# Kernel tuning notes

Hardware: AMD Instinct MI355X
Metric: run time of the kernel (lower is better)

The kernel has to match this reference:

```python
import jax, jax.numpy as jnp
import numpy as np

DELTA = 10.0
EPS = 1e-08
THRESHOLD = 0.9
STEEPNESS = 10.0


def setup_inputs() -> dict:
    key = jax.random.key(0)
    k1, k2 = jax.random.split(key)
    B, T2, T1, F = 16, 2048, 512, 128
    mels = jax.random.normal(k1, (B, T2, F), dtype=jnp.float32)
    alpha = jax.random.uniform(k2, (B, T2, T1), dtype=jnp.float32)
    mel_mask = jnp.ones((B, T2), dtype=jnp.int32)
    text_mask = jnp.ones((B, T1), dtype=jnp.int32)
    return {"mels": mels, "alpha": alpha, "mel_mask": mel_mask, "text_mask": text_mask}


def reference(mels, alpha, mel_mask, text_mask):
    B, T2, F = mels.shape
    T1 = text_mask.shape[-1]
    audio_mask = mel_mask.astype(bool)
    txt_mask = text_mask.astype(bool)
    am_f = audio_mask.astype(alpha.dtype)  # [B, T2]
    tm_f = txt_mask.astype(alpha.dtype)    # [B, T1]

    # index vector p: [B, T1]
    p = jnp.broadcast_to(jnp.arange(T1, dtype=alpha.dtype), (B, T1))

    # cosine similarity between consecutive frames (F.normalize: x / max(||x||, 1e-12))
    norm = jnp.maximum(jnp.linalg.norm(mels, axis=-1, keepdims=True), 1e-12)
    z_norm = mels / norm
    cosine_sim = jnp.sum(z_norm[:, :-1] * z_norm[:, 1:], axis=-1)  # [B, T2-1]
    activity = jax.nn.sigmoid(STEEPNESS * (THRESHOLD - cosine_sim))
    activity = jnp.concatenate([jnp.ones((B, 1), dtype=activity.dtype), activity], axis=-1)
    activity = activity * am_f

    # soft monotonic index via gated cumsum of alpha-proposal increments
    imv_proposal = jnp.einsum('bts,bs->bt', alpha, p)  # [B, T2]
    delta_prop = jnp.concatenate(
        [jnp.zeros((B, 1), dtype=imv_proposal.dtype), jnp.diff(imv_proposal, axis=-1)], axis=-1)
    eff_delta = jnp.clip(delta_prop * activity, 0.0, 1.0)
    imv = jnp.cumsum(eff_delta, axis=-1) * am_f

    # rescale so last valid frame maps to last phoneme index
    last_idx = jnp.maximum(audio_mask.sum(-1).astype(jnp.int32) - 1, 0)  # [B]
    last_val = jnp.maximum(jnp.take_along_axis(imv, last_idx[:, None], axis=1)[:, 0], 1e-06)
    text_len = txt_mask.sum(-1).astype(imv.dtype)
    scale = jnp.maximum(text_len - 1.0, 0.0) / last_val
    imv = imv * scale[:, None] * am_f

    # gamma: masked softmax over phonemes of -delta * (imv - p)^2
    dist_sq = (imv[:, :, None] - p[:, None, :]) ** 2  # [B, T2, T1]
    logits = jnp.where(txt_mask[:, None, :], -DELTA * dist_sq, -1e9)
    gamma = jax.nn.softmax(logits, axis=-1) * am_f[:, :, None]

    # durations: soft mass per phoneme
    durations = jnp.sum(gamma * am_f[:, :, None], axis=1) * tm_f  # [B, T1]

    # attention-pooling of mel frames onto phonemes
    w = jnp.swapaxes(gamma, 1, 2) * am_f[:, None, :]  # [B, T1, T2]
    w = w / (jnp.sum(w, axis=-1, keepdims=True) + EPS)
    aligned_mels = jnp.einsum('bst,btf->bsf', w, mels) * tm_f[:, :, None]  # [B, T1, F]
    return aligned_mels, durations, imv
```

## Files before the change

kernel.cpp:

```cpp
#include <hip/hip_runtime.h>
#include <math.h>
#include <cstddef>

#define B_  16
#define T2_ 2048
#define T1_ 512
#define F_  128

constexpr float DELTA_C  = 10.0f;
constexpr float EPS_C    = 1e-8f;
constexpr float THRESH_C = 0.9f;
constexpr float STEEP_C  = 10.0f;

__global__ __launch_bounds__(256) void actprop_kernel(const float* __restrict__ mels,
                                                      const float* __restrict__ alpha,
                                                      const int* __restrict__ mel_mask,
                                                      float* __restrict__ act,
                                                      float* __restrict__ prop) {
    int wid  = (int)((blockIdx.x * blockDim.x + threadIdx.x) >> 6);
    int lane = threadIdx.x & 63;
    if (wid >= B_ * T2_) return;
    int t = wid % T2_;

    const float4* row = (const float4*)(alpha + (size_t)wid * T1_);
    float4 v0 = row[lane];
    float4 v1 = row[lane + 64];

    float d = 0.f, n0 = 0.f, n1 = 0.f;
    if (t > 0) {
        float2 x = ((const float2*)(mels + (size_t)(wid - 1) * F_))[lane];
        float2 y = ((const float2*)(mels + (size_t)wid * F_))[lane];
        d  = x.x * y.x + x.y * y.y;
        n0 = x.x * x.x + x.y * x.y;
        n1 = y.x * y.x + y.y * y.y;
    }

    float fL = (float)(lane * 4);
    float psum = v0.x * fL + v0.y * (fL + 1.f) + v0.z * (fL + 2.f) + v0.w * (fL + 3.f)
               + v1.x * (fL + 256.f) + v1.y * (fL + 257.f) + v1.z * (fL + 258.f) + v1.w * (fL + 259.f);

    for (int off = 32; off > 0; off >>= 1) {
        psum += __shfl_xor(psum, off, 64);
        d    += __shfl_xor(d,    off, 64);
        n0   += __shfl_xor(n0,   off, 64);
        n1   += __shfl_xor(n1,   off, 64);
    }

    if (lane == 0) {
        float a_val;
        if (t == 0) {
            a_val = 1.0f;
        } else {
            float cs = d / (fmaxf(sqrtf(n0), 1e-12f) * fmaxf(sqrtf(n1), 1e-12f));
            a_val = 1.0f / (1.0f + __expf(-STEEP_C * (THRESH_C - cs)));
        }
        act[wid]  = a_val * (float)mel_mask[wid];
        prop[wid] = psum;
    }
}

__global__ __launch_bounds__(256) void scan_kernel(const float* __restrict__ prop,
                                                   const float* __restrict__ act,
                                                   const int* __restrict__ mel_mask,
                                                   const int* __restrict__ text_mask,
                                                   float* __restrict__ imv_out,
                                                   float2* __restrict__ packed) {
    int b    = blockIdx.x;
    int tid  = threadIdx.x;
    int wave = tid >> 6, lane = tid & 63;
    __shared__ float s_imv[T2_];
    __shared__ float s_part[256];
    __shared__ int   s_am4[4], s_tm4[4];

    const float* pr = prop + (size_t)b * T2_;
    const float* ac = act  + (size_t)b * T2_;
    const int*   mm = mel_mask  + (size_t)b * T2_;
    const int*   tm = text_mask + (size_t)b * T1_;

    float e[8];
    int t0 = tid * 8;
    int am_local = 0;
    float run = 0.0f;
    for (int i = 0; i < 8; i++) {
        int t = t0 + i;
        float d = (t == 0) ? 0.0f : (pr[t] - pr[t - 1]) * ac[t];
        d = fminf(fmaxf(d, 0.0f), 1.0f);
        run += d;
        e[i] = run;
        am_local += mm[t];
    }
    int tm_local = tm[tid] + tm[tid + 256];
    for (int off = 32; off > 0; off >>= 1) {
        am_local += __shfl_xor(am_local, off, 64);
        tm_local += __shfl_xor(tm_local, off, 64);
    }
    if (lane == 0) { s_am4[wave] = am_local; s_tm4[wave] = tm_local; }
    s_part[tid] = run;
    __syncthreads();

    for (int off = 1; off < 256; off <<= 1) {
        float u = (tid >= off) ? s_part[tid - off] : 0.0f;
        __syncthreads();
        s_part[tid] += u;
        __syncthreads();
    }
    float excl = (tid == 0) ? 0.0f : s_part[tid - 1];
    for (int i = 0; i < 8; i++) {
        int t = t0 + i;
        s_imv[t] = (e[i] + excl) * (float)mm[t];
    }
    __syncthreads();

    int am_total = s_am4[0] + s_am4[1] + s_am4[2] + s_am4[3];
    int tm_total = s_tm4[0] + s_tm4[1] + s_tm4[2] + s_tm4[3];
    int last_idx = max(am_total - 1, 0);
    float last_val = fmaxf(s_imv[last_idx], 1e-6f);
    float scale = fmaxf((float)tm_total - 1.0f, 0.0f) / last_val;

    for (int i = 0; i < 8; i++) {
        int t = t0 + i;
        int valid = mm[t];
        float v = s_imv[t] * scale * (float)valid;
        imv_out[(size_t)b * T2_ + t] = v;
        int c = (int)floorf(v);
        float Z = 0.0f;
        for (int s = c - 2; s <= c + 3; s++) {
            if (s >= 0 && s < T1_ && tm[s]) {
                float dd = v - (float)s;
                Z += __expf(-DELTA_C * dd * dd);
            }
        }
        Z = fmaxf(Z, 1e-30f);
        float2 pk;
        pk.x = valid ? v : 3.0e4f;
        pk.y = valid ? (1.0f / Z) : 0.0f;
        packed[(size_t)b * T2_ + t] = pk;
    }
}

__global__ __launch_bounds__(256) void pool_kernel(const float* __restrict__ mels,
                                                   const int* __restrict__ text_mask,
                                                   const float2* __restrict__ packed,
                                                   float* __restrict__ aligned,
                                                   float* __restrict__ dur) {
    int wid  = (int)((blockIdx.x * blockDim.x + threadIdx.x) >> 6);
    int lane = threadIdx.x & 63;
    if (wid >= B_ * T1_) return;
    int b = wid / T1_, s = wid % T1_;
    const float2* pk   = packed + (size_t)b * T2_;
    const float2* mel2 = (const float2*)(mels + (size_t)b * T2_ * F_);

    float fs = (float)s;
    float lo_v = fs - 3.0f, hi_v = fs + 3.0f;
    int lo = 0, hi = T2_;
    while (lo < hi) { int mid = (lo + hi) >> 1; if (pk[mid].x >= lo_v) hi = mid; else lo = mid + 1; }
    int t_lo = lo;
    hi = T2_;
    while (lo < hi) { int mid = (lo + hi) >> 1; if (pk[mid].x > hi_v) hi = mid; else lo = mid + 1; }
    int t_hi = lo;

    float ax = 0.0f, ay = 0.0f, gsum = 0.0f;
    int t = t_lo;
    for (; t + 4 <= t_hi; t += 4) {
        float2 p0 = pk[t], p1 = pk[t + 1], p2 = pk[t + 2], p3 = pk[t + 3];
        float2 m0 = mel2[(size_t)(t    ) * 64 + lane];
        float2 m1 = mel2[(size_t)(t + 1) * 64 + lane];
        float2 m2 = mel2[(size_t)(t + 2) * 64 + lane];
        float2 m3 = mel2[(size_t)(t + 3) * 64 + lane];
        float d0 = p0.x - fs, d1 = p1.x - fs, d2 = p2.x - fs, d3 = p3.x - fs;
        float g0 = __expf(-DELTA_C * d0 * d0) * p0.y;
        float g1 = __expf(-DELTA_C * d1 * d1) * p1.y;
        float g2 = __expf(-DELTA_C * d2 * d2) * p2.y;
        float g3 = __expf(-DELTA_C * d3 * d3) * p3.y;
        gsum += (g0 + g1) + (g2 + g3);
        ax += g0 * m0.x + g1 * m1.x + g2 * m2.x + g3 * m3.x;
        ay += g0 * m0.y + g1 * m1.y + g2 * m2.y + g3 * m3.y;
    }
    for (; t < t_hi; t++) {
        float2 p = pk[t];
        float2 m = mel2[(size_t)t * 64 + lane];
        float dd = p.x - fs;
        float g  = __expf(-DELTA_C * dd * dd) * p.y;
        gsum += g;
        ax += g * m.x;
        ay += g * m.y;
    }

    float tmv = (float)text_mask[(size_t)b * T1_ + s];
    float inv = tmv / (gsum + EPS_C);
    float2 outv = {ax * inv, ay * inv};
    ((float2*)(aligned + ((size_t)b * T1_ + s) * F_))[lane] = outv;
    if (lane == 0) dur[(size_t)b * T1_ + s] = gsum * tmv;
}

extern "C" void kernel_launch(void* const* d_in, const int* in_sizes, int n_in,
                              void* d_out, int out_size, void* d_ws, size_t ws_size,
                              hipStream_t stream) {
    const float* mels      = (const float*)d_in[0];
    const float* alpha     = (const float*)d_in[1];
    const int*   mel_mask  = (const int*)d_in[2];
    const int*   text_mask = (const int*)d_in[3];

    float* out     = (float*)d_out;
    float* aligned = out;
    float* dur     = out + (size_t)B_ * T1_ * F_;
    float* imv     = dur + (size_t)B_ * T1_;

    float*  ws     = (float*)d_ws;
    float*  act    = ws;
    float*  prop   = ws + (size_t)B_ * T2_;
    float2* packed = (float2*)(ws + 2 * (size_t)B_ * T2_);

    dim3 blk(256);
    actprop_kernel<<<(B_ * T2_) / 4, blk, 0, stream>>>(mels, alpha, mel_mask, act, prop);
    scan_kernel   <<<B_,            blk, 0, stream>>>(prop, act, mel_mask, text_mask, imv, packed);
    pool_kernel   <<<(B_ * T1_) / 4, blk, 0, stream>>>(mels, text_mask, packed, aligned, dur);
}
```

Measured before the change: 134.3 us.

## Precompute pooling bounds in scan, wave-shuffle scan, pool two phonemes per wave

The scan kernel now uses a wave-level shuffle prefix scan instead of a multi-barrier shared-memory scan. It caches masks in shared memory and registers, and computes each phoneme's frame window with binary search in shared memory, writing the bounds to the workspace. The pool kernel reads these bounds and processes two adjacent phonemes per wave, so mel rows are loaded once for both. Alpha is read with nontemporal loads. This adds workspace usage and more work per wave in the scan kernel.

```diff
diff --git a/kernel.cpp b/kernel.cpp
--- a/kernel.cpp
+++ b/kernel.cpp
@@ -11,6 +11,8 @@
 constexpr float EPS_C    = 1e-8f;
 constexpr float THRESH_C = 0.9f;
 constexpr float STEEP_C  = 10.0f;
+
+typedef float f4v __attribute__((ext_vector_type(4)));
 
 __global__ __launch_bounds__(256) void actprop_kernel(const float* __restrict__ mels,
                                                       const float* __restrict__ alpha,
@@ -22,9 +24,9 @@
     if (wid >= B_ * T2_) return;
     int t = wid % T2_;
 
-    const float4* row = (const float4*)(alpha + (size_t)wid * T1_);
-    float4 v0 = row[lane];
-    float4 v1 = row[lane + 64];
+    const f4v* row = (const f4v*)(alpha + (size_t)wid * T1_);
+    f4v v0 = __builtin_nontemporal_load(&row[lane]);
+    f4v v1 = __builtin_nontemporal_load(&row[lane + 64]);
 
     float d = 0.f, n0 = 0.f, n1 = 0.f;
     if (t > 0) {
@@ -64,20 +66,26 @@
                                                    const int* __restrict__ mel_mask,
                                                    const int* __restrict__ text_mask,
                                                    float* __restrict__ imv_out,
-                                                   float2* __restrict__ packed) {
+                                                   float2* __restrict__ packed,
+                                                   int2* __restrict__ bounds) {
     int b    = blockIdx.x;
     int tid  = threadIdx.x;
     int wave = tid >> 6, lane = tid & 63;
     __shared__ float s_imv[T2_];
-    __shared__ float s_part[256];
+    __shared__ float s_wsum[4];
     __shared__ int   s_am4[4], s_tm4[4];
+    __shared__ int   s_tm[T1_];
 
     const float* pr = prop + (size_t)b * T2_;
     const float* ac = act  + (size_t)b * T2_;
     const int*   mm = mel_mask  + (size_t)b * T2_;
     const int*   tm = text_mask + (size_t)b * T1_;
 
+    int tmv0 = tm[tid], tmv1 = tm[tid + 256];
+    s_tm[tid] = tmv0; s_tm[tid + 256] = tmv1;
+
     float e[8];
+    int   mmv[8];
     int t0 = tid * 8;
     int am_local = 0;
     float run = 0.0f;
@@ -87,27 +95,30 @@
         d = fminf(fmaxf(d, 0.0f), 1.0f);
         run += d;
         e[i] = run;
-        am_local += mm[t];
-    }
-    int tm_local = tm[tid] + tm[tid + 256];
+        mmv[i] = mm[t];
+        am_local += mmv[i];
+    }
+    int tm_local = tmv0 + tmv1;
     for (int off = 32; off > 0; off >>= 1) {
         am_local += __shfl_xor(am_local, off, 64);
         tm_local += __shfl_xor(tm_local, off, 64);
     }
     if (lane == 0) { s_am4[wave] = am_local; s_tm4[wave] = tm_local; }
-    s_part[tid] = run;
-    __syncthreads();
-
-    for (int off = 1; off < 256; off <<= 1) {
-        float u = (tid >= off) ? s_part[tid - off] : 0.0f;
-        __syncthreads();
-        s_part[tid] += u;
-        __syncthreads();
-    }
-    float excl = (tid == 0) ? 0.0f : s_part[tid - 1];
+
+    float v = run;
+    for (int off = 1; off < 64; off <<= 1) {
+        float u = __shfl_up(v, off, 64);
+        if (lane >= off) v += u;
+    }
+    if (lane == 63) s_wsum[wave] = v;
+    __syncthreads();
+
+    float woff = 0.0f;
+    for (int w = 0; w < 4; w++) woff += (w < wave) ? s_wsum[w] : 0.0f;
+    float excl = woff + v - run;
     for (int i = 0; i < 8; i++) {
         int t = t0 + i;
-        s_imv[t] = (e[i] + excl) * (float)mm[t];
+        s_imv[t] = (e[i] + excl) * (float)mmv[i];
     }
     __syncthreads();
 
@@ -116,81 +127,100 @@
     int last_idx = max(am_total - 1, 0);
     float last_val = fmaxf(s_imv[last_idx], 1e-6f);
     float scale = fmaxf((float)tm_total - 1.0f, 0.0f) / last_val;
+    __syncthreads();
 
     for (int i = 0; i < 8; i++) {
         int t = t0 + i;
-        int valid = mm[t];
-        float v = s_imv[t] * scale * (float)valid;
-        imv_out[(size_t)b * T2_ + t] = v;
-        int c = (int)floorf(v);
+        int valid = mmv[i];
+        float vv = s_imv[t] * scale * (float)valid;
+        imv_out[(size_t)b * T2_ + t] = vv;
+        int c = (int)floorf(vv);
         float Z = 0.0f;
         for (int s = c - 2; s <= c + 3; s++) {
-            if (s >= 0 && s < T1_ && tm[s]) {
-                float dd = v - (float)s;
+            if (s >= 0 && s < T1_ && s_tm[s]) {
+                float dd = vv - (float)s;
                 Z += __expf(-DELTA_C * dd * dd);
             }
         }
         Z = fmaxf(Z, 1e-30f);
-        float2 pk;
-        pk.x = valid ? v : 3.0e4f;
-        pk.y = valid ? (1.0f / Z) : 0.0f;
+        float key = valid ? vv : 3.0e4f;
+        float2 pk = {key, valid ? (1.0f / Z) : 0.0f};
         packed[(size_t)b * T2_ + t] = pk;
+        s_imv[t] = key;
+    }
+    __syncthreads();
+
+    for (int k = 0; k < 2; k++) {
+        int s = tid + k * 256;
+        float lov = (float)s - 3.0f, hiv = (float)s + 3.0f;
+        int lo = 0, hi = T2_;
+        while (lo < hi) { int mid = (lo + hi) >> 1; if (s_imv[mid] >= lov) hi = mid; else lo = mid + 1; }
+        int st = lo;
+        hi = T2_;
+        while (lo < hi) { int mid = (lo + hi) >> 1; if (s_imv[mid] > hiv) hi = mid; else lo = mid + 1; }
+        int2 be = {st, lo};
+        bounds[(size_t)b * T1_ + s] = be;
     }
 }
 
 __global__ __launch_bounds__(256) void pool_kernel(const float* __restrict__ mels,
                                                    const int* __restrict__ text_mask,
                                                    const float2* __restrict__ packed,
+                                                   const int2* __restrict__ bounds,
                                                    float* __restrict__ aligned,
                                                    float* __restrict__ dur) {
     int wid  = (int)((blockIdx.x * blockDim.x + threadIdx.x) >> 6);
     int lane = threadIdx.x & 63;
-    if (wid >= B_ * T1_) return;
-    int b = wid / T1_, s = wid % T1_;
+    if (wid >= B_ * (T1_ / 2)) return;
+    int b = wid >> 8, s0 = (wid & 255) * 2;
+    float fs0 = (float)s0, fs1 = fs0 + 1.0f;
+
     const float2* pk   = packed + (size_t)b * T2_;
     const float2* mel2 = (const float2*)(mels + (size_t)b * T2_ * F_);
-
-    float fs = (float)s;
-    float lo_v = fs - 3.0f, hi_v = fs + 3.0f;
-    int lo = 0, hi = T2_;
-    while (lo < hi) { int mid = (lo + hi) >> 1; if (pk[mid].x >= lo_v) hi = mid; else lo = mid + 1; }
-    int t_lo = lo;
-    hi = T2_;
-    while (lo < hi) { int mid = (lo + hi) >> 1; if (pk[mid].x > hi_v) hi = mid; else lo = mid + 1; }
-    int t_hi = lo;
-
-    float ax = 0.0f, ay = 0.0f, gsum = 0.0f;
+    int2 b0 = bounds[(size_t)b * T1_ + s0];
+    int2 b1 = bounds[(size_t)b * T1_ + s0 + 1];
+    int t_lo = b0.x, t_hi = b1.y;
+
+    float ax0 = 0.f, ay0 = 0.f, g0s = 0.f;
+    float ax1 = 0.f, ay1 = 0.f, g1s = 0.f;
     int t = t_lo;
-    for (; t + 4 <= t_hi; t += 4) {
-        float2 p0 = pk[t], p1 = pk[t + 1], p2 = pk[t + 2], p3 = pk[t + 3];
-        float2 m0 = mel2[(size_t)(t    ) * 64 + lane];
+    for (; t + 2 <= t_hi; t += 2) {
+        float2 p0 = pk[t], p1 = pk[t + 1];
+        float2 m0 = mel2[(size_t)t * 64 + lane];
         float2 m1 = mel2[(size_t)(t + 1) * 64 + lane];
-        float2 m2 = mel2[(size_t)(t + 2) * 64 + lane];
-        float2 m3 = mel2[(size_t)(t + 3) * 64 + lane];
-        float d0 = p0.x - fs, d1 = p1.x - fs, d2 = p2.x - fs, d3 = p3.x - fs;
-        float g0 = __expf(-DELTA_C * d0 * d0) * p0.y;
-        float g1 = __expf(-DELTA_C * d1 * d1) * p1.y;
-        float g2 = __expf(-DELTA_C * d2 * d2) * p2.y;
-        float g3 = __expf(-DELTA_C * d3 * d3) * p3.y;
-        gsum += (g0 + g1) + (g2 + g3);
-        ax += g0 * m0.x + g1 * m1.x + g2 * m2.x + g3 * m3.x;
-        ay += g0 * m0.y + g1 * m1.y + g2 * m2.y + g3 * m3.y;
+        float d00 = p0.x - fs0, d01 = p0.x - fs1;
+        float d10 = p1.x - fs0, d11 = p1.x - fs1;
+        float g00 = __expf(-DELTA_C * d00 * d00) * p0.y;
+        float g01 = __expf(-DELTA_C * d01 * d01) * p0.y;
+        float g10 = __expf(-DELTA_C * d10 * d10) * p1.y;
+        float g11 = __expf(-DELTA_C * d11 * d11) * p1.y;
+        g0s += g00 + g10; g1s += g01 + g11;
+        ax0 += g00 * m0.x + g10 * m1.x;  ay0 += g00 * m0.y + g10 * m1.y;
+        ax1 += g01 * m0.x + g11 * m1.x;  ay1 += g01 * m0.y + g11 * m1.y;
     }
     for (; t < t_hi; t++) {
         float2 p = pk[t];
         float2 m = mel2[(size_t)t * 64 + lane];
-        float dd = p.x - fs;
-        float g  = __expf(-DELTA_C * dd * dd) * p.y;
-        gsum += g;
-        ax += g * m.x;
-        ay += g * m.y;
-    }
-
-    float tmv = (float)text_mask[(size_t)b * T1_ + s];
-    float inv = tmv / (gsum + EPS_C);
-    float2 outv = {ax * inv, ay * inv};
-    ((float2*)(aligned + ((size_t)b * T1_ + s) * F_))[lane] = outv;
-    if (lane == 0) dur[(size_t)b * T1_ + s] = gsum * tmv;
+        float d0 = p.x - fs0, d1 = p.x - fs1;
+        float ga = __expf(-DELTA_C * d0 * d0) * p.y;
+        float gb = __expf(-DELTA_C * d1 * d1) * p.y;
+        g0s += ga; g1s += gb;
+        ax0 += ga * m.x; ay0 += ga * m.y;
+        ax1 += gb * m.x; ay1 += gb * m.y;
+    }
+
+    float tm0 = (float)text_mask[(size_t)b * T1_ + s0];
+    float tm1 = (float)text_mask[(size_t)b * T1_ + s0 + 1];
+    float inv0 = tm0 / (g0s + EPS_C);
+    float inv1 = tm1 / (g1s + EPS_C);
+    float2 o0 = {ax0 * inv0, ay0 * inv0};
+    float2 o1 = {ax1 * inv1, ay1 * inv1};
+    ((float2*)(aligned + ((size_t)b * T1_ + s0) * F_))[lane] = o0;
+    ((float2*)(aligned + ((size_t)b * T1_ + s0 + 1) * F_))[lane] = o1;
+    if (lane == 0) {
+        dur[(size_t)b * T1_ + s0]     = g0s * tm0;
+        dur[(size_t)b * T1_ + s0 + 1] = g1s * tm1;
+    }
 }
 
 extern "C" void kernel_launch(void* const* d_in, const int* in_sizes, int n_in,
@@ -210,9 +240,10 @@
     float*  act    = ws;
     float*  prop   = ws + (size_t)B_ * T2_;
     float2* packed = (float2*)(ws + 2 * (size_t)B_ * T2_);
+    int2*   bounds = (int2*)(ws + 4 * (size_t)B_ * T2_);
 
     dim3 blk(256);
     actprop_kernel<<<(B_ * T2_) / 4, blk, 0, stream>>>(mels, alpha, mel_mask, act, prop);
-    scan_kernel   <<<B_,            blk, 0, stream>>>(prop, act, mel_mask, text_mask, imv, packed);
-    pool_kernel   <<<(B_ * T1_) / 4, blk, 0, stream>>>(mels, text_mask, packed, aligned, dur);
-}
+    scan_kernel   <<<B_,            blk, 0, stream>>>(prop, act, mel_mask, text_mask, imv, packed, bounds);
+    pool_kernel   <<<(B_ * T1_ / 2) / 4, blk, 0, stream>>>(mels, text_mask, packed, bounds, aligned, dur);
+}
```

New measurement: 133.1 us. Within noise of the previous version (-0.9%).
